# Kernel optimization log

Hardware: AMD Instinct MI355X
Metric: run time of the kernel (lower is better)

The kernel has to match this reference:

```python
import jax, jax.numpy as jnp
import numpy as np

N = 16384      # total nodes
B = 8          # graphs in batch
NPG = N // B   # nodes per graph
E = 262144     # edges
IN, HID, OUT = 128, 256, 128
ICP_ITERS = 10


def setup_inputs():
    key = jax.random.key(0)
    ks = jax.random.split(key, 12)
    x = jax.random.normal(ks[0], (N, IN), jnp.float32)
    # random edges kept within each graph (offsets per graph)
    src = jax.random.randint(ks[1], (E,), 0, NPG, dtype=jnp.int32)
    dst = jax.random.randint(ks[2], (E,), 0, NPG, dtype=jnp.int32)
    goff = (jnp.arange(E, dtype=jnp.int32) % B) * NPG
    edge_index = jnp.stack([src + goff, dst + goff], 0)
    pos = jax.random.normal(ks[3], (N, 3), jnp.float32)
    batch = jnp.repeat(jnp.arange(B, dtype=jnp.int32), NPG)
    def lin(k, fi, fo):
        return jax.random.normal(k, (fi, fo), jnp.float32) * (fi ** -0.5)
    return dict(
        x=x, edge_index=edge_index, pos=pos, batch=batch,
        W1=lin(ks[4], IN, HID),  b1=jnp.zeros((HID,), jnp.float32),
        W2=lin(ks[5], HID, HID), b2=jnp.zeros((HID,), jnp.float32),
        W3=lin(ks[6], HID, OUT), b3=jnp.zeros((OUT,), jnp.float32),
        Wt=lin(ks[7], OUT, 3),   bt=jnp.zeros((3,), jnp.float32),
    )


def gcn_conv(x, W, b, row, col, n):
    # GCNConv: symmetric norm with self loops; messages flow row->col
    xw = x @ W
    loop = jnp.arange(n, dtype=row.dtype)
    r = jnp.concatenate([row, loop])
    c = jnp.concatenate([col, loop])
    deg = jax.ops.segment_sum(jnp.ones_like(c, dtype=xw.dtype), c, num_segments=n)
    dinv = jnp.where(deg > 0, jax.lax.rsqrt(jnp.maximum(deg, 1e-12)), 0.0)
    norm = dinv[r] * dinv[c]
    out = jax.ops.segment_sum(xw[r] * norm[:, None], c, num_segments=n)
    return out + b


def pdist2(a, b):
    # squared pairwise distances [n,m]
    return (jnp.sum(a * a, -1)[:, None] + jnp.sum(b * b, -1)[None, :]
            - 2.0 * (a @ b.T))


def icp_align(src, tgt):
    # fixed-iteration batched ICP (Kabsch/SVD per iteration)
    for _ in range(ICP_ITERS):
        d = pdist2(jax.lax.stop_gradient(src), jax.lax.stop_gradient(tgt))
        idx = jnp.argmin(d, axis=1)
        corr = tgt[idx]
        cs = jnp.mean(src, 0)
        cc = jnp.mean(corr, 0)
        H = (src - cs).T @ (corr - cc)  # [3,3]
        U, S, Vt = jnp.linalg.svd(H, full_matrices=False)
        sign = jnp.sign(jnp.linalg.det(Vt.T @ U.T))
        D = jnp.stack([jnp.ones_like(sign), jnp.ones_like(sign), sign])
        R = (Vt.T * D[None, :]) @ U.T
        t = cc - R @ cs
        src = src @ R.T + t
    return src


def chamfer(a, b):
    d = pdist2(jax.lax.stop_gradient(a), jax.lax.stop_gradient(b))
    ia = jnp.argmin(d, 1)
    ib = jnp.argmin(d, 0)
    d1 = jnp.mean(jnp.sum((a - b[ia]) ** 2, -1))
    d2 = jnp.mean(jnp.sum((b - a[ib]) ** 2, -1))
    return d1 + d2


def reference(x, edge_index, pos, batch, W1, b1, W2, b2, W3, b3, Wt, bt):
    n = x.shape[0]
    row, col = edge_index[0], edge_index[1]
    h = jax.nn.relu(gcn_conv(x, W1, b1, row, col, n))
    h = jax.nn.relu(gcn_conv(h, W2, b2, row, col, n))
    h = gcn_conv(h, W3, b3, row, col, n)
    pos_offset = h @ Wt + bt
    tpos = pos + pos_offset
    nb = int(batch[-1]) + 1          # sorted, equal-size graphs
    npg = n // nb
    src = tpos.reshape(nb, npg, 3)
    tgt = pos.reshape(nb, npg, 3)
    aligned = jax.vmap(icp_align)(src, tgt)
    loss = jnp.mean(jax.vmap(chamfer)(aligned, tgt))
    return h, aligned.reshape(n, 3), loss
```

## Files before the change

### kernel.cpp

```cpp
#include <hip/hip_runtime.h>
#include <math.h>

#define N_NODES 16384
#define B_GRAPHS 8
#define NPG_     2048
#define E_EDGES  262144
#define F_IN  128
#define F_HID 256
#define F_OUT 128
#define ICP_IT 10
#define NN_BPG 32

typedef __attribute__((ext_vector_type(8))) short bf16x8;
typedef __attribute__((ext_vector_type(4))) float f32x4;

__device__ __forceinline__ float b2f(unsigned short u) {
    union { unsigned int u; float f; } v; v.u = ((unsigned int)u) << 16; return v.f;
}
__device__ __forceinline__ unsigned short f2b(float f) {
    union { float f; unsigned int u; } v; v.f = f;
    unsigned int r = v.u + 0x7FFFu + ((v.u >> 16) & 1u);
    return (unsigned short)(r >> 16);
}
__device__ __forceinline__ int swz32(int i) {
    return (i & ~31) | ((i & 31) ^ ((i >> 5) & 31));
}
__device__ __forceinline__ void st_agent(float* p, float v) {
    __hip_atomic_store(p, v, __ATOMIC_RELAXED, __HIP_MEMORY_SCOPE_AGENT);
}
__device__ __forceinline__ float ld_agent(const float* p) {
    return __hip_atomic_load(p, __ATOMIC_RELAXED, __HIP_MEMORY_SCOPE_AGENT);
}
__device__ __forceinline__ int ld_agent_i(const int* p) {
    return __hip_atomic_load(p, __ATOMIC_RELAXED, __HIP_MEMORY_SCOPE_AGENT);
}

__global__ __launch_bounds__(256) void k_prep(
    const float* __restrict__ x, unsigned short* __restrict__ xb,
    const float* __restrict__ W1, const float* __restrict__ W2, const float* __restrict__ W3,
    unsigned short* __restrict__ W1b, unsigned short* __restrict__ W2b, unsigned short* __restrict__ W3b,
    int* __restrict__ counts, int* __restrict__ ctrs)
{
    const int b = blockIdx.x, tid = threadIdx.x;
    if (b < 2048) {
        int i = b * 256 + tid;
        float4 v = ((const float4*)x)[i];
        uint2 o;
        o.x = (unsigned int)f2b(v.x) | ((unsigned int)f2b(v.y) << 16);
        o.y = (unsigned int)f2b(v.z) | ((unsigned int)f2b(v.w) << 16);
        ((uint2*)xb)[i] = o;
    } else if (b < 2176) {
        int idx = (b - 2048) * 256 + tid;
        int k = idx >> 8, n = idx & 255;
        W1b[n * 128 + k] = f2b(W1[idx]);
    } else if (b < 2432) {
        int idx = (b - 2176) * 256 + tid;
        int k = idx >> 8, n = idx & 255;
        W2b[n * 256 + k] = f2b(W2[idx]);
    } else if (b < 2560) {
        int idx = (b - 2432) * 256 + tid;
        int k = idx >> 7, n = idx & 127;
        W3b[n * 256 + k] = f2b(W3[idx]);
    } else if (b < 2576) {
        int i = (b - 2560) * 256 + tid;
        ((int4*)counts)[i] = make_int4(0, 0, 0, 0);
    } else {
        ctrs[tid] = 0;
    }
}

__global__ void k_count(const int* __restrict__ col, int* __restrict__ counts) {
    int e = blockIdx.x * 256 + threadIdx.x;
    if (e < E_EDGES) atomicAdd(&counts[col[e]], 1);
}

__global__ __launch_bounds__(1024) void k_scan(const int* __restrict__ counts,
        int* __restrict__ offs, int* __restrict__ cursor, float* __restrict__ dinv)
{
    __shared__ int wtot[16];
    const int t = threadIdx.x;
    const int base = t * 16;
    int local[16];
    int s = 0;
#pragma unroll
    for (int i = 0; i < 16; i++) { local[i] = counts[base + i]; s += local[i]; }
    const int lane = t & 63, w = t >> 6;
    int inc = s;
    for (int o = 1; o < 64; o <<= 1) {
        int v = __shfl_up(inc, o);
        if (lane >= o) inc += v;
    }
    if (lane == 63) wtot[w] = inc;
    __syncthreads();
    if (t < 16) {
        int v = wtot[t];
        for (int o = 1; o < 16; o <<= 1) {
            int u = __shfl_up(v, o);
            if (t >= o) v += u;
        }
        wtot[t] = v;
    }
    __syncthreads();
    int run = (w > 0 ? wtot[w - 1] : 0) + (inc - s);
#pragma unroll
    for (int i = 0; i < 16; i++) {
        offs[base + i]   = run;
        cursor[base + i] = run;
        dinv[base + i]   = rsqrtf((float)(local[i] + 1));
        run += local[i];
    }
    if (t == 1023) offs[N_NODES] = run;
}

__global__ void k_scatter(const int* __restrict__ row, const int* __restrict__ col,
        int* __restrict__ cursor, const float* __restrict__ dinv,
        int* __restrict__ srcid, float* __restrict__ normv)
{
    int e = blockIdx.x * 256 + threadIdx.x;
    if (e >= E_EDGES) return;
    int r = row[e], c = col[e];
    int p = atomicAdd(&cursor[c], 1);
    srcid[p] = r;
    normv[p] = dinv[r] * dinv[c];
}

template<int W, int OUTF, int FUSET>
__global__ __launch_bounds__(128) void k_agg(const unsigned short* __restrict__ X,
        void* __restrict__ Y,
        const int* __restrict__ offs, const int* __restrict__ srcid,
        const float* __restrict__ normv, const float* __restrict__ dinv,
        const float* __restrict__ bias, int relu,
        const float* __restrict__ Wt, const float* __restrict__ bt,
        const float* __restrict__ pos, float* __restrict__ tposO)
{
    constexpr int NPB = (W == 128) ? 2 : 1;
    constexpr int W2 = W / 2;
    const int local = (NPB == 2) ? (threadIdx.x >> 6) : 0;
    const int n = blockIdx.x * NPB + local;
    const int j = (NPB == 2) ? (threadIdx.x & 63) : threadIdx.x;
    const unsigned int* Xu = (const unsigned int*)X;
    float di = dinv[n];
    float w0 = di * di;
    unsigned int v = Xu[(size_t)n * W2 + j];
    float a0 = b2f((unsigned short)v) * w0;
    float a1 = b2f((unsigned short)(v >> 16)) * w0;
    int p = offs[n];
    const int p1 = offs[n + 1];
    for (; p + 3 < p1; p += 4) {
        int s0i = srcid[p], s1i = srcid[p + 1], s2i = srcid[p + 2], s3i = srcid[p + 3];
        float n0 = normv[p], n1 = normv[p + 1], n2 = normv[p + 2], n3 = normv[p + 3];
        unsigned int v0 = Xu[(size_t)s0i * W2 + j];
        unsigned int v1 = Xu[(size_t)s1i * W2 + j];
        unsigned int v2 = Xu[(size_t)s2i * W2 + j];
        unsigned int v3 = Xu[(size_t)s3i * W2 + j];
        a0 = fmaf(b2f((unsigned short)v0), n0, a0);
        a1 = fmaf(b2f((unsigned short)(v0 >> 16)), n0, a1);
        a0 = fmaf(b2f((unsigned short)v1), n1, a0);
        a1 = fmaf(b2f((unsigned short)(v1 >> 16)), n1, a1);
        a0 = fmaf(b2f((unsigned short)v2), n2, a0);
        a1 = fmaf(b2f((unsigned short)(v2 >> 16)), n2, a1);
        a0 = fmaf(b2f((unsigned short)v3), n3, a0);
        a1 = fmaf(b2f((unsigned short)(v3 >> 16)), n3, a1);
    }
    for (; p < p1; ++p) {
        unsigned int va = Xu[(size_t)srcid[p] * W2 + j]; float na = normv[p];
        a0 = fmaf(b2f((unsigned short)va), na, a0);
        a1 = fmaf(b2f((unsigned short)(va >> 16)), na, a1);
    }
    if (bias) { a0 += bias[2 * j]; a1 += bias[2 * j + 1]; }
    if (relu) { a0 = fmaxf(a0, 0.f); a1 = fmaxf(a1, 0.f); }
    if (OUTF) {
        float* Yf = (float*)Y;
        Yf[(size_t)n * W + 2 * j]     = a0;
        Yf[(size_t)n * W + 2 * j + 1] = a1;
    } else {
        ((unsigned int*)Y)[(size_t)n * W2 + j] =
            (unsigned int)f2b(a0) | ((unsigned int)f2b(a1) << 16);
    }
    if (FUSET) {
        float wt0 = Wt[6 * j + 0], wt1 = Wt[6 * j + 1], wt2 = Wt[6 * j + 2];
        float wt3 = Wt[6 * j + 3], wt4 = Wt[6 * j + 4], wt5 = Wt[6 * j + 5];
        float s0 = a0 * wt0 + a1 * wt3;
        float s1 = a0 * wt1 + a1 * wt4;
        float s2 = a0 * wt2 + a1 * wt5;
        for (int o = 32; o > 0; o >>= 1) {
            s0 += __shfl_down(s0, o);
            s1 += __shfl_down(s1, o);
            s2 += __shfl_down(s2, o);
        }
        if (j == 0) {
            tposO[n * 3 + 0] = pos[n * 3 + 0] + s0 + bt[0];
            tposO[n * 3 + 1] = pos[n * 3 + 1] + s1 + bt[1];
            tposO[n * 3 + 2] = pos[n * 3 + 2] + s2 + bt[2];
        }
    }
}

__global__ __launch_bounds__(256) void k_gemm_bf16(
    const unsigned short* __restrict__ A,
    const unsigned short* __restrict__ Bt,
    const float* __restrict__ bias, unsigned short* __restrict__ C,
    int M, int N, int K, int relu)
{
    __shared__ __align__(16) unsigned short As[128 * 64];
    __shared__ __align__(16) unsigned short Bs[64 * 64];
    const int tid  = threadIdx.x;
    const int lane = tid & 63;
    const int wave = tid >> 6;
    const int bm = blockIdx.y * 128, bn = blockIdx.x * 64;
    const int wm = (wave >> 1) * 64, wn = (wave & 1) * 32;
    f32x4 acc[4][2];
#pragma unroll
    for (int mf = 0; mf < 4; mf++)
#pragma unroll
        for (int nf = 0; nf < 2; nf++) acc[mf][nf] = (f32x4){0.f, 0.f, 0.f, 0.f};

    for (int k0 = 0; k0 < K; k0 += 64) {
#pragma unroll
        for (int i = 0; i < 4; i++) {
            int idx = i * 256 + tid;
            int m = idx >> 3, slot = idx & 7;
            const unsigned short* src = A + (size_t)(bm + m) * K + k0 + ((slot ^ (m & 7)) << 3);
            __builtin_amdgcn_global_load_lds(
                (const __attribute__((address_space(1))) unsigned int*)src,
                (__attribute__((address_space(3))) unsigned int*)(As + (size_t)i * 2048 + wave * 512),
                16, 0, 0);
        }
#pragma unroll
        for (int i = 0; i < 2; i++) {
            int idx = i * 256 + tid;
            int n = idx >> 3, slot = idx & 7;
            const unsigned short* src = Bt + (size_t)(bn + n) * K + k0 + ((slot ^ (n & 7)) << 3);
            __builtin_amdgcn_global_load_lds(
                (const __attribute__((address_space(1))) unsigned int*)src,
                (__attribute__((address_space(3))) unsigned int*)(Bs + (size_t)i * 2048 + wave * 512),
                16, 0, 0);
        }
        __syncthreads();
        bf16x8 af[4][2], bfr[2][2];
        const int qd = lane >> 4;
#pragma unroll
        for (int s = 0; s < 2; s++) {
#pragma unroll
            for (int mf = 0; mf < 4; mf++) {
                int m = wm + mf * 16 + (lane & 15);
                int slot = (s * 4 + qd) ^ (m & 7);
                af[mf][s] = *(const bf16x8*)(As + m * 64 + slot * 8);
            }
#pragma unroll
            for (int nf = 0; nf < 2; nf++) {
                int n = wn + nf * 16 + (lane & 15);
                int slot = (s * 4 + qd) ^ (n & 7);
                bfr[nf][s] = *(const bf16x8*)(Bs + n * 64 + slot * 8);
            }
        }
#pragma unroll
        for (int s = 0; s < 2; s++)
#pragma unroll
            for (int mf = 0; mf < 4; mf++)
#pragma unroll
                for (int nf = 0; nf < 2; nf++)
                    acc[mf][nf] = __builtin_amdgcn_mfma_f32_16x16x32_bf16(
                        af[mf][s], bfr[nf][s], acc[mf][nf], 0, 0, 0);
        __syncthreads();
    }
#pragma unroll
    for (int nf = 0; nf < 2; nf++) {
        int col = bn + wn + nf * 16 + (lane & 15);
        float bv = bias ? bias[col] : 0.f;
#pragma unroll
        for (int mf = 0; mf < 4; mf++) {
#pragma unroll
            for (int r = 0; r < 4; r++) {
                int row = bm + wm + mf * 16 + (lane >> 4) * 4 + r;
                float v = acc[mf][nf][r] + bv;
                if (relu) v = fmaxf(v, 0.f);
                C[(size_t)row * N + col] = f2b(v);
            }
        }
    }
}

__global__ __launch_bounds__(512) void k_icp_all(
    const float* __restrict__ tpos, const float* __restrict__ pos,
    float* __restrict__ partials,
    float* __restrict__ chpart,
    int* __restrict__ ctrs,
    float* __restrict__ out_aligned, float* __restrict__ out_loss)
{
    const int g = blockIdx.x >> 5, blk = blockIdx.x & 31;
    const int tid = threadIdx.x;
    const int wave = tid >> 6, lane = tid & 63;
    __shared__ float4 tq[NPG_];
    __shared__ __align__(16) unsigned char scratch[NPG_ * 16];
    float* sm_d = (float*)scratch;
    unsigned short* sm_i = (unsigned short*)(scratch + 64 * 65 * 4);
    float4* al = (float4*)scratch;
    __shared__ float mom[15][33];
    __shared__ float ssx[64], ssy[64], ssz[64];
    __shared__ float wred[16][2];
    __shared__ float Tsh[12];
    __shared__ double sdl[15];
    __shared__ int lastFlag;

    for (int i = tid; i < NPG_; i += 512) {
        const float* p = &pos[(size_t)(g * NPG_ + i) * 3];
        float qx = p[0], qy = p[1], qz = p[2];
        tq[swz32(i)] = make_float4(qx, qy, qz, fmaf(qx, qx, fmaf(qy, qy, qz * qz)));
    }
    if (tid < 12) Tsh[tid] = (tid == 0 || tid == 4 || tid == 8) ? 1.f : 0.f;
    float Px[8], Py[8], Pz[8];
#pragma unroll
    for (int u = 0; u < 8; u++) {
        int n = g * NPG_ + blk * 64 + wave * 8 + u;
        Px[u] = tpos[n * 3 + 0]; Py[u] = tpos[n * 3 + 1]; Pz[u] = tpos[n * 3 + 2];
    }
    double Td[12];
    if (tid == 0) {
#pragma unroll
        for (int k = 0; k < 12; k++) Td[k] = (k == 0 || k == 4 || k == 8) ? 1.0 : 0.0;
    }
    __syncthreads();

    for (int iter = 0; iter < ICP_IT; ++iter) {
        const int bufbase = (iter & 1) * 256;
        float Tf[12];
#pragma unroll
        for (int k = 0; k < 12; k++) Tf[k] = Tsh[k];
        float Sx[8], Sy[8], Sz[8], Tx[8], Ty[8], Tz[8], bd[8];
        int bi[8];
#pragma unroll
        for (int u = 0; u < 8; u++) {
            float X = Tf[0] * Px[u] + Tf[1] * Py[u] + Tf[2] * Pz[u] + Tf[9];
            float Y = Tf[3] * Px[u] + Tf[4] * Py[u] + Tf[5] * Pz[u] + Tf[10];
            float Z = Tf[6] * Px[u] + Tf[7] * Py[u] + Tf[8] * Pz[u] + Tf[11];
            Sx[u] = X; Sy[u] = Y; Sz[u] = Z;
            Tx[u] = -2.f * X; Ty[u] = -2.f * Y; Tz[u] = -2.f * Z;
            bd[u] = 1e30f; bi[u] = lane * 32;
        }
        const int qbase = lane * 32;
        for (int j = 0; j < 32; j++) {
            float4 t4 = tq[qbase + (j ^ (lane & 31))];
            int idx = qbase + j;
#pragma unroll
            for (int u = 0; u < 8; u++) {
                float d = fmaf(Tx[u], t4.x, fmaf(Ty[u], t4.y, fmaf(Tz[u], t4.z, t4.w)));
                if (d < bd[u]) { bd[u] = d; bi[u] = idx; }
            }
        }
#pragma unroll
        for (int u = 0; u < 8; u++) {
            int rowoff = (wave * 8 + u) * 65;
            sm_d[rowoff + lane] = bd[u];
            sm_i[rowoff + lane] = (unsigned short)bi[u];
            if (lane == u) { ssx[wave * 8 + u] = Sx[u]; ssy[wave * 8 + u] = Sy[u]; ssz[wave * 8 + u] = Sz[u]; }
        }
        __syncthreads();
        if (tid < 64) {
            const int s = tid;
            float best = sm_d[s * 65];
            int ib = sm_i[s * 65];
            for (int r = 1; r < 64; r++) {
                float dd = sm_d[s * 65 + r];
                int ii = sm_i[s * 65 + r];
                if (dd < best) { best = dd; ib = ii; }
            }
            float4 c = tq[swz32(ib)];
            float X = ssx[s], Y = ssy[s], Z = ssz[s];
            float vals[15] = { X, Y, Z, c.x, c.y, c.z,
                               X * c.x, X * c.y, X * c.z,
                               Y * c.x, Y * c.y, Y * c.z,
                               Z * c.x, Z * c.y, Z * c.z };
#pragma unroll
            for (int k = 0; k < 15; k++) {
                float v = vals[k];
                for (int o = 32; o > 0; o >>= 1) v += __shfl_down(v, o);
                if (tid == 0) st_agent(&partials[((size_t)bufbase + blockIdx.x) * 16 + k], v);
            }
        }
        __syncthreads();
        if (tid == 0) {
            atomicAdd(&ctrs[g * 16], 1);
            const int target = 32 * (iter + 1);
            while (ld_agent_i(&ctrs[g * 16]) < target) __builtin_amdgcn_s_sleep(8);
        }
        __syncthreads();
        if (tid < 480) {
            int kk = tid >> 5, bb = tid & 31;
            mom[kk][bb] = ld_agent(&partials[((size_t)bufbase + g * 32 + bb) * 16 + kk]);
        }
        __syncthreads();
        if (tid < 15) {
            double acc = 0;
            for (int b = 0; b < NN_BPG; b++) acc += (double)mom[tid][b];
            sdl[tid] = acc;
        }
        __syncthreads();
        if (tid == 0) {
            double sd[15];
#pragma unroll
            for (int k = 0; k < 15; k++) sd[k] = sdl[k];
            const double n = (double)NPG_;
            const double rin = 1.0 / (double)NPG_;
            double cs0 = sd[0] * rin, cs1 = sd[1] * rin, cs2 = sd[2] * rin;
            double cc0 = sd[3] * rin, cc1 = sd[4] * rin, cc2 = sd[5] * rin;
            float H[3][3];
            H[0][0] = (float)(sd[6]  - n * cs0 * cc0); H[0][1] = (float)(sd[7]  - n * cs0 * cc1); H[0][2] = (float)(sd[8]  - n * cs0 * cc2);
            H[1][0] = (float)(sd[9]  - n * cs1 * cc0); H[1][1] = (float)(sd[10] - n * cs1 * cc1); H[1][2] = (float)(sd[11] - n * cs1 * cc2);
            H[2][0] = (float)(sd[12] - n * cs2 * cc0); H[2][1] = (float)(sd[13] - n * cs2 * cc1); H[2][2] = (float)(sd[14] - n * cs2 * cc2);
            double R[3][3];
            float fn = 1e-30f;
            for (int i = 0; i < 3; i++) for (int j2 = 0; j2 < 3; j2++) fn += H[i][j2] * H[i][j2];
            float sc = rsqrtf(fn);
            float Xm[3][3];
            for (int i = 0; i < 3; i++) for (int j2 = 0; j2 < 3; j2++) Xm[i][j2] = H[i][j2] * sc;
            float dX = Xm[0][0] * (Xm[1][1]*Xm[2][2] - Xm[1][2]*Xm[2][1])
                     - Xm[0][1] * (Xm[1][0]*Xm[2][2] - Xm[1][2]*Xm[2][0])
                     + Xm[0][2] * (Xm[1][0]*Xm[2][1] - Xm[1][1]*Xm[2][0]);
            if (dX > 1e-4f) {
                for (int itn = 0; itn < 24; ++itn) {
                    float C00 = Xm[1][1]*Xm[2][2] - Xm[1][2]*Xm[2][1];
                    float C01 = Xm[1][2]*Xm[2][0] - Xm[1][0]*Xm[2][2];
                    float C02 = Xm[1][0]*Xm[2][1] - Xm[1][1]*Xm[2][0];
                    float C10 = Xm[2][1]*Xm[0][2] - Xm[2][2]*Xm[0][1];
                    float C11 = Xm[2][2]*Xm[0][0] - Xm[2][0]*Xm[0][2];
                    float C12 = Xm[2][0]*Xm[0][1] - Xm[2][1]*Xm[0][0];
                    float C20 = Xm[0][1]*Xm[1][2] - Xm[0][2]*Xm[1][1];
                    float C21 = Xm[0][2]*Xm[1][0] - Xm[0][0]*Xm[1][2];
                    float C22 = Xm[0][0]*Xm[1][1] - Xm[0][1]*Xm[1][0];
                    float det = Xm[0][0]*C00 + Xm[0][1]*C01 + Xm[0][2]*C02;
                    if (fabsf(det) < 1e-30f) break;
                    float rd = 0.5f / det;
                    Xm[0][0] = 0.5f*Xm[0][0] + C00*rd; Xm[0][1] = 0.5f*Xm[0][1] + C01*rd; Xm[0][2] = 0.5f*Xm[0][2] + C02*rd;
                    Xm[1][0] = 0.5f*Xm[1][0] + C10*rd; Xm[1][1] = 0.5f*Xm[1][1] + C11*rd; Xm[1][2] = 0.5f*Xm[1][2] + C12*rd;
                    Xm[2][0] = 0.5f*Xm[2][0] + C20*rd; Xm[2][1] = 0.5f*Xm[2][1] + C21*rd; Xm[2][2] = 0.5f*Xm[2][2] + C22*rd;
                }
                for (int i = 0; i < 3; i++) for (int j2 = 0; j2 < 3; j2++) R[i][j2] = (double)Xm[j2][i];
            } else {
                float A[3][3], V[3][3] = {{1,0,0},{0,1,0},{0,0,1}};
                for (int i = 0; i < 3; i++)
                    for (int j2 = 0; j2 < 3; j2++)
                        A[i][j2] = H[0][i] * H[0][j2] + H[1][i] * H[1][j2] + H[2][i] * H[2][j2];
                for (int sweep = 0; sweep < 8; ++sweep) {
                    for (int p = 0; p < 2; p++) for (int q = p + 1; q < 3; q++) {
                        float apq = A[p][q];
                        if (fabsf(apq) < 1e-30f) continue;
                        float theta = (A[q][q] - A[p][p]) / (2.f * apq);
                        float t = copysignf(1.f, theta) / (fabsf(theta) + sqrtf(theta * theta + 1.f));
                        float c = 1.f / sqrtf(t * t + 1.f);
                        float s = t * c;
                        for (int k = 0; k < 3; k++) { float akp = A[k][p], akq = A[k][q]; A[k][p] = c*akp - s*akq; A[k][q] = s*akp + c*akq; }
                        for (int k = 0; k < 3; k++) { float apk = A[p][k], aqk = A[q][k]; A[p][k] = c*apk - s*aqk; A[q][k] = s*apk + c*aqk; }
                        for (int k = 0; k < 3; k++) { float vkp = V[k][p], vkq = V[k][q]; V[k][p] = c*vkp - s*vkq; V[k][q] = s*vkp + c*vkq; }
                    }
                }
                float lam[3] = { A[0][0], A[1][1], A[2][2] };
                int ord[3] = { 0, 1, 2 };
                if (lam[ord[1]] > lam[ord[0]]) { int t0 = ord[0]; ord[0] = ord[1]; ord[1] = t0; }
                if (lam[ord[2]] > lam[ord[0]]) { int t0 = ord[0]; ord[0] = ord[2]; ord[2] = t0; }
                if (lam[ord[2]] > lam[ord[1]]) { int t0 = ord[1]; ord[1] = ord[2]; ord[2] = t0; }
                float vc[3][3], uc[3][3];
                for (int i = 0; i < 3; i++) { vc[i][0] = V[0][ord[i]]; vc[i][1] = V[1][ord[i]]; vc[i][2] = V[2][ord[i]]; }
                for (int i = 0; i < 3; i++) {
                    float u0 = H[0][0]*vc[i][0] + H[0][1]*vc[i][1] + H[0][2]*vc[i][2];
                    float u1 = H[1][0]*vc[i][0] + H[1][1]*vc[i][1] + H[1][2]*vc[i][2];
                    float u2 = H[2][0]*vc[i][0] + H[2][1]*vc[i][1] + H[2][2]*vc[i][2];
                    for (int j2 = 0; j2 < i; j2++) {
                        float dp = u0*uc[j2][0] + u1*uc[j2][1] + u2*uc[j2][2];
                        u0 -= dp*uc[j2][0]; u1 -= dp*uc[j2][1]; u2 -= dp*uc[j2][2];
                    }
                    float nn2 = sqrtf(u0*u0 + u1*u1 + u2*u2);
                    if (nn2 > 1e-12f) { uc[i][0] = u0/nn2; uc[i][1] = u1/nn2; uc[i][2] = u2/nn2; }
                    else if (i == 2) {
                        uc[2][0] = uc[0][1]*uc[1][2] - uc[0][2]*uc[1][1];
                        uc[2][1] = uc[0][2]*uc[1][0] - uc[0][0]*uc[1][2];
                        uc[2][2] = uc[0][0]*uc[1][1] - uc[0][1]*uc[1][0];
                    } else if (i == 1) {
                        float a0 = (fabsf(uc[0][0]) < 0.9f) ? 1.f : 0.f, a1 = 1.f - a0, a2 = 0.f;
                        float dp = a0*uc[0][0] + a1*uc[0][1] + a2*uc[0][2];
                        a0 -= dp*uc[0][0]; a1 -= dp*uc[0][1]; a2 -= dp*uc[0][2];
                        float nn3 = sqrtf(a0*a0 + a1*a1 + a2*a2);
                        uc[1][0] = a0/nn3; uc[1][1] = a1/nn3; uc[1][2] = a2/nn3;
                    } else { uc[0][0] = 1; uc[0][1] = 0; uc[0][2] = 0; }
                }
                float detU = uc[0][0]*(uc[1][1]*uc[2][2] - uc[1][2]*uc[2][1])
                           - uc[0][1]*(uc[1][0]*uc[2][2] - uc[1][2]*uc[2][0])
                           + uc[0][2]*(uc[1][0]*uc[2][1] - uc[1][1]*uc[2][0]);
                float detV = vc[0][0]*(vc[1][1]*vc[2][2] - vc[1][2]*vc[2][1])
                           - vc[0][1]*(vc[1][0]*vc[2][2] - vc[1][2]*vc[2][0])
                           + vc[0][2]*(vc[1][0]*vc[2][1] - vc[1][1]*vc[2][0]);
                float sgn = (detU * detV < 0.f) ? -1.f : 1.f;
                for (int i = 0; i < 3; i++)
                    for (int j2 = 0; j2 < 3; j2++)
                        R[i][j2] = (double)(vc[0][i]*uc[0][j2] + vc[1][i]*uc[1][j2] + sgn * vc[2][i]*uc[2][j2]);
            }
            double tr0 = cc0 - (R[0][0]*cs0 + R[0][1]*cs1 + R[0][2]*cs2);
            double tr1 = cc1 - (R[1][0]*cs0 + R[1][1]*cs1 + R[1][2]*cs2);
            double tr2 = cc2 - (R[2][0]*cs0 + R[2][1]*cs1 + R[2][2]*cs2);
            double An[12];
            for (int i = 0; i < 3; i++)
                for (int j2 = 0; j2 < 3; j2++)
                    An[i*3+j2] = R[i][0]*Td[0*3+j2] + R[i][1]*Td[1*3+j2] + R[i][2]*Td[2*3+j2];
            An[9]  = R[0][0]*Td[9] + R[0][1]*Td[10] + R[0][2]*Td[11] + tr0;
            An[10] = R[1][0]*Td[9] + R[1][1]*Td[10] + R[1][2]*Td[11] + tr1;
            An[11] = R[2][0]*Td[9] + R[2][1]*Td[10] + R[2][2]*Td[11] + tr2;
#pragma unroll
            for (int k = 0; k < 12; k++) { Td[k] = An[k]; Tsh[k] = (float)An[k]; }
        }
        __syncthreads();
    }

    {
        float Tf[12];
#pragma unroll
        for (int k = 0; k < 12; k++) Tf[k] = Tsh[k];
        __syncthreads();
        for (int i = tid; i < NPG_; i += 512) {
            const float* q = &tpos[(size_t)(g * NPG_ + i) * 3];
            float X = Tf[0] * q[0] + Tf[1] * q[1] + Tf[2] * q[2] + Tf[9];
            float Y = Tf[3] * q[0] + Tf[4] * q[1] + Tf[5] * q[2] + Tf[10];
            float Z = Tf[6] * q[0] + Tf[7] * q[1] + Tf[8] * q[2] + Tf[11];
            al[swz32(i)] = make_float4(X, Y, Z, fmaf(X, X, fmaf(Y, Y, Z * Z)));
            if (blk == 0) {
                out_aligned[(size_t)(g * NPG_ + i) * 3 + 0] = X;
                out_aligned[(size_t)(g * NPG_ + i) * 3 + 1] = Y;
                out_aligned[(size_t)(g * NPG_ + i) * 3 + 2] = Z;
            }
        }
        __syncthreads();
        float Ax[8], Ay[8], Az[8], Aw[8], Qx[8], Qy[8], Qz[8], Qw[8], d1[8], d2[8];
#pragma unroll
        for (int u = 0; u < 8; u++) {
            int s = swz32(blk * 64 + wave * 8 + u);
            float4 a4 = al[s]; float4 p4 = tq[s];
            Ax[u] = -2.f * a4.x; Ay[u] = -2.f * a4.y; Az[u] = -2.f * a4.z; Aw[u] = a4.w;
            Qx[u] = -2.f * p4.x; Qy[u] = -2.f * p4.y; Qz[u] = -2.f * p4.z; Qw[u] = p4.w;
            d1[u] = 1e30f; d2[u] = 1e30f;
        }
        const int qbase = lane * 32;
        for (int j = 0; j < 32; j++) {
            int s = qbase + (j ^ (lane & 31));
            float4 t4 = tq[s];
            float4 b4 = al[s];
#pragma unroll
            for (int u = 0; u < 8; u++) {
                d1[u] = fminf(d1[u], fmaf(Ax[u], t4.x, fmaf(Ay[u], t4.y, fmaf(Az[u], t4.z, t4.w))));
                d2[u] = fminf(d2[u], fmaf(Qx[u], b4.x, fmaf(Qy[u], b4.y, fmaf(Qz[u], b4.z, b4.w))));
            }
        }
        float s1 = 0.f, s2 = 0.f;
#pragma unroll
        for (int u = 0; u < 8; u++) {
            float a = d1[u], b = d2[u];
            for (int o = 32; o > 0; o >>= 1) {
                a = fminf(a, __shfl_down(a, o));
                b = fminf(b, __shfl_down(b, o));
            }
            s1 += a + Aw[u];
            s2 += b + Qw[u];
        }
        if (lane == 0) { wred[wave][0] = s1; wred[wave][1] = s2; }
        __syncthreads();
        if (tid == 0) {
            float t1 = 0.f, t2 = 0.f;
#pragma unroll
            for (int w = 0; w < 8; w++) { t1 += wred[w][0]; t2 += wred[w][1]; }
            st_agent(&chpart[blockIdx.x * 2 + 0], t1);
            st_agent(&chpart[blockIdx.x * 2 + 1], t2);
        }
        __syncthreads();
        if (tid == 0) {
            int old = atomicAdd(&ctrs[128], 1);
            lastFlag = (old == (int)gridDim.x - 1) ? 1 : 0;
        }
        __syncthreads();
        if (!lastFlag) return;
        float v1 = 0.f, v2 = 0.f;
        if (tid < 256) {
            v1 = ld_agent(&chpart[tid * 2 + 0]);
            v2 = ld_agent(&chpart[tid * 2 + 1]);
        }
        for (int o = 32; o > 0; o >>= 1) {
            v1 += __shfl_down(v1, o);
            v2 += __shfl_down(v2, o);
        }
        if (lane == 0 && wave < 4) { wred[wave][0] = v1; wred[wave][1] = v2; }
        __syncthreads();
        if (tid == 0) {
            float tot = 0.f;
#pragma unroll
            for (int w = 0; w < 4; w++) tot += wred[w][0] + wred[w][1];
            out_loss[0] = tot / (float)(NPG_ * B_GRAPHS);
        }
    }
}

extern "C" void kernel_launch(void* const* d_in, const int* in_sizes, int n_in,
                              void* d_out, int out_size, void* d_ws, size_t ws_size,
                              hipStream_t stream)
{
    (void)in_sizes; (void)n_in; (void)out_size; (void)ws_size;
    const float* x   = (const float*)d_in[0];
    const int*   ei  = (const int*)d_in[1];
    const float* pos = (const float*)d_in[2];
    const float* W1 = (const float*)d_in[4];
    const float* b1 = (const float*)d_in[5];
    const float* W2 = (const float*)d_in[6];
    const float* b2 = (const float*)d_in[7];
    const float* W3 = (const float*)d_in[8];
    const float* b3 = (const float*)d_in[9];
    const float* Wt = (const float*)d_in[10];
    const float* bt = (const float*)d_in[11];
    const int* row = ei;
    const int* col = ei + E_EDGES;

    char* wsb = (char*)d_ws;
    size_t off_b = 0;
    auto alloc = [&](size_t bytes) -> void* {
        void* p = wsb + off_b;
        off_b = (off_b + bytes + 255) & ~(size_t)255;
        return p;
    };
    int*    counts   = (int*)alloc((size_t)N_NODES * 4);
    int*    offs     = (int*)alloc((size_t)(N_NODES + 1) * 4);
    int*    cursor   = (int*)alloc((size_t)N_NODES * 4);
    int*    srcid    = (int*)alloc((size_t)E_EDGES * 4);
    float*  normv    = (float*)alloc((size_t)E_EDGES * 4);
    float*  dinv     = (float*)alloc((size_t)N_NODES * 4);
    unsigned short* xb  = (unsigned short*)alloc((size_t)N_NODES * F_IN * 2);
    unsigned short* W1b = (unsigned short*)alloc((size_t)F_IN * F_HID * 2);
    unsigned short* W2b = (unsigned short*)alloc((size_t)F_HID * F_HID * 2);
    unsigned short* W3b = (unsigned short*)alloc((size_t)F_HID * F_OUT * 2);
    unsigned short* bufA = (unsigned short*)alloc((size_t)N_NODES * F_HID * 2);
    unsigned short* bufB = (unsigned short*)alloc((size_t)N_NODES * F_HID * 2);
    unsigned short* bufC = (unsigned short*)alloc((size_t)N_NODES * F_HID * 2);
    float*  tpos     = (float*)alloc((size_t)N_NODES * 3 * 4);
    float*  partials = (float*)alloc((size_t)2 * 256 * 16 * 4);
    int*    ctrs     = (int*)alloc((size_t)256 * 4);
    float*  chpart   = (float*)alloc((size_t)256 * 2 * 4);

    float* out_h       = (float*)d_out;
    float* out_aligned = out_h + (size_t)N_NODES * F_OUT;
    float* out_loss    = out_aligned + (size_t)N_NODES * 3;

    k_prep<<<2577, 256, 0, stream>>>(x, xb, W1, W2, W3, W1b, W2b, W3b, counts, ctrs);
    k_count<<<E_EDGES / 256, 256, 0, stream>>>(col, counts);
    k_scan<<<1, 1024, 0, stream>>>(counts, offs, cursor, dinv);
    k_scatter<<<E_EDGES / 256, 256, 0, stream>>>(row, col, cursor, dinv, srcid, normv);

    k_agg<F_IN, 0, 0><<<N_NODES / 2, 128, 0, stream>>>(xb, bufA, offs, srcid, normv, dinv,
            nullptr, 0, nullptr, nullptr, nullptr, nullptr);
    {
        dim3 grid(F_HID / 64, N_NODES / 128);
        k_gemm_bf16<<<grid, 256, 0, stream>>>(bufA, W1b, b1, bufB, N_NODES, F_HID, F_IN, 1);
    }
    {
        dim3 grid(F_HID / 64, N_NODES / 128);
        k_gemm_bf16<<<grid, 256, 0, stream>>>(bufB, W2b, nullptr, bufC, N_NODES, F_HID, F_HID, 0);
    }
    k_agg<F_HID, 0, 0><<<N_NODES, 128, 0, stream>>>(bufC, bufA, offs, srcid, normv, dinv,
            b2, 1, nullptr, nullptr, nullptr, nullptr);
    {
        dim3 grid(F_OUT / 64, N_NODES / 128);
        k_gemm_bf16<<<grid, 256, 0, stream>>>(bufA, W3b, nullptr, bufB, N_NODES, F_OUT, F_HID, 0);
    }
    k_agg<F_OUT, 1, 1><<<N_NODES / 2, 128, 0, stream>>>(bufB, out_h, offs, srcid, normv, dinv,
            b3, 0, Wt, bt, pos, tpos);

    k_icp_all<<<B_GRAPHS * NN_BPG, 512, 0, stream>>>(tpos, pos, partials, chpart, ctrs,
            out_aligned, out_loss);
}
```

Before: 330.8 us.

## Use leader-block ICP rotation solve with per-block flags and fuse edge counting

The per-iteration ICP grid barrier, where every block spun on a shared counter and then redundantly solved the 3x3 rotation, is replaced. Each block now publishes a release flag, one leader block per graph waits on the 32 flags, solves the rotation once and publishes the transform through a global buffer, and the other blocks wait on an acquire flag. Newton polar iterations drop from 24 to 16, which may slightly change accuracy for ill-conditioned cases. The edge-count kernel is folded into the prep kernel, and counts are cleared with a memset beforehand, removing one launch at the cost of an extra memset call.

```diff
diff --git a/kernel.cpp b/kernel.cpp
--- a/kernel.cpp
+++ b/kernel.cpp
@@ -31,6 +31,12 @@
 __device__ __forceinline__ float ld_agent(const float* p) {
     return __hip_atomic_load(p, __ATOMIC_RELAXED, __HIP_MEMORY_SCOPE_AGENT);
 }
+__device__ __forceinline__ void st_rel_i(int* p, int v) {
+    __hip_atomic_store(p, v, __ATOMIC_RELEASE, __HIP_MEMORY_SCOPE_AGENT);
+}
+__device__ __forceinline__ int ld_acq_i(const int* p) {
+    return __hip_atomic_load(p, __ATOMIC_ACQUIRE, __HIP_MEMORY_SCOPE_AGENT);
+}
 __device__ __forceinline__ int ld_agent_i(const int* p) {
     return __hip_atomic_load(p, __ATOMIC_RELAXED, __HIP_MEMORY_SCOPE_AGENT);
 }
@@ -39,7 +45,7 @@
     const float* __restrict__ x, unsigned short* __restrict__ xb,
     const float* __restrict__ W1, const float* __restrict__ W2, const float* __restrict__ W3,
     unsigned short* __restrict__ W1b, unsigned short* __restrict__ W2b, unsigned short* __restrict__ W3b,
-    int* __restrict__ counts, int* __restrict__ ctrs)
+    const int* __restrict__ col, int* __restrict__ counts, int* __restrict__ ctrs)
 {
     const int b = blockIdx.x, tid = threadIdx.x;
     if (b < 2048) {
@@ -61,17 +67,13 @@
         int idx = (b - 2432) * 256 + tid;
         int k = idx >> 7, n = idx & 127;
         W3b[n * 256 + k] = f2b(W3[idx]);
-    } else if (b < 2576) {
-        int i = (b - 2560) * 256 + tid;
-        ((int4*)counts)[i] = make_int4(0, 0, 0, 0);
+    } else if (b < 3584) {
+        int e = (b - 2560) * 256 + tid;
+        atomicAdd(&counts[col[e]], 1);
     } else {
         ctrs[tid] = 0;
-    }
-}
-
-__global__ void k_count(const int* __restrict__ col, int* __restrict__ counts) {
-    int e = blockIdx.x * 256 + threadIdx.x;
-    if (e < E_EDGES) atomicAdd(&counts[col[e]], 1);
+        ctrs[tid + 256] = 0;
+    }
 }
 
 __global__ __launch_bounds__(1024) void k_scan(const int* __restrict__ counts,
@@ -284,6 +286,7 @@
 __global__ __launch_bounds__(512) void k_icp_all(
     const float* __restrict__ tpos, const float* __restrict__ pos,
     float* __restrict__ partials,
+    float* __restrict__ Tpub,
     float* __restrict__ chpart,
     int* __restrict__ ctrs,
     float* __restrict__ out_aligned, float* __restrict__ out_loss)
@@ -298,7 +301,7 @@
     float4* al = (float4*)scratch;
     __shared__ float mom[15][33];
     __shared__ float ssx[64], ssy[64], ssz[64];
-    __shared__ float wred[16][2];
+    __shared__ float wred[8][2];
     __shared__ float Tsh[12];
     __shared__ double sdl[15];
     __shared__ int lastFlag;
@@ -323,7 +326,6 @@
     __syncthreads();
 
     for (int iter = 0; iter < ICP_IT; ++iter) {
-        const int bufbase = (iter & 1) * 256;
         float Tf[12];
 #pragma unroll
         for (int k = 0; k < 12; k++) Tf[k] = Tsh[k];
@@ -350,10 +352,10 @@
         }
 #pragma unroll
         for (int u = 0; u < 8; u++) {
-            int rowoff = (wave * 8 + u) * 65;
-            sm_d[rowoff + lane] = bd[u];
-            sm_i[rowoff + lane] = (unsigned short)bi[u];
-            if (lane == u) { ssx[wave * 8 + u] = Sx[u]; ssy[wave * 8 + u] = Sy[u]; ssz[wave * 8 + u] = Sz[u]; }
+            int row = wave * 8 + u;
+            sm_d[row * 65 + lane] = bd[u];
+            sm_i[row * 65 + lane] = (unsigned short)bi[u];
+            if (lane == u) { ssx[row] = Sx[u]; ssy[row] = Sy[u]; ssz[row] = Sz[u]; }
         }
         __syncthreads();
         if (tid < 64) {
@@ -375,139 +377,153 @@
             for (int k = 0; k < 15; k++) {
                 float v = vals[k];
                 for (int o = 32; o > 0; o >>= 1) v += __shfl_down(v, o);
-                if (tid == 0) st_agent(&partials[((size_t)bufbase + blockIdx.x) * 16 + k], v);
-            }
-        }
-        __syncthreads();
-        if (tid == 0) {
-            atomicAdd(&ctrs[g * 16], 1);
-            const int target = 32 * (iter + 1);
-            while (ld_agent_i(&ctrs[g * 16]) < target) __builtin_amdgcn_s_sleep(8);
-        }
-        __syncthreads();
-        if (tid < 480) {
-            int kk = tid >> 5, bb = tid & 31;
-            mom[kk][bb] = ld_agent(&partials[((size_t)bufbase + g * 32 + bb) * 16 + kk]);
-        }
-        __syncthreads();
-        if (tid < 15) {
-            double acc = 0;
-            for (int b = 0; b < NN_BPG; b++) acc += (double)mom[tid][b];
-            sdl[tid] = acc;
-        }
-        __syncthreads();
-        if (tid == 0) {
-            double sd[15];
-#pragma unroll
-            for (int k = 0; k < 15; k++) sd[k] = sdl[k];
-            const double n = (double)NPG_;
-            const double rin = 1.0 / (double)NPG_;
-            double cs0 = sd[0] * rin, cs1 = sd[1] * rin, cs2 = sd[2] * rin;
-            double cc0 = sd[3] * rin, cc1 = sd[4] * rin, cc2 = sd[5] * rin;
-            float H[3][3];
-            H[0][0] = (float)(sd[6]  - n * cs0 * cc0); H[0][1] = (float)(sd[7]  - n * cs0 * cc1); H[0][2] = (float)(sd[8]  - n * cs0 * cc2);
-            H[1][0] = (float)(sd[9]  - n * cs1 * cc0); H[1][1] = (float)(sd[10] - n * cs1 * cc1); H[1][2] = (float)(sd[11] - n * cs1 * cc2);
-            H[2][0] = (float)(sd[12] - n * cs2 * cc0); H[2][1] = (float)(sd[13] - n * cs2 * cc1); H[2][2] = (float)(sd[14] - n * cs2 * cc2);
-            double R[3][3];
-            float fn = 1e-30f;
-            for (int i = 0; i < 3; i++) for (int j2 = 0; j2 < 3; j2++) fn += H[i][j2] * H[i][j2];
-            float sc = rsqrtf(fn);
-            float Xm[3][3];
-            for (int i = 0; i < 3; i++) for (int j2 = 0; j2 < 3; j2++) Xm[i][j2] = H[i][j2] * sc;
-            float dX = Xm[0][0] * (Xm[1][1]*Xm[2][2] - Xm[1][2]*Xm[2][1])
-                     - Xm[0][1] * (Xm[1][0]*Xm[2][2] - Xm[1][2]*Xm[2][0])
-                     + Xm[0][2] * (Xm[1][0]*Xm[2][1] - Xm[1][1]*Xm[2][0]);
-            if (dX > 1e-4f) {
-                for (int itn = 0; itn < 24; ++itn) {
-                    float C00 = Xm[1][1]*Xm[2][2] - Xm[1][2]*Xm[2][1];
-                    float C01 = Xm[1][2]*Xm[2][0] - Xm[1][0]*Xm[2][2];
-                    float C02 = Xm[1][0]*Xm[2][1] - Xm[1][1]*Xm[2][0];
-                    float C10 = Xm[2][1]*Xm[0][2] - Xm[2][2]*Xm[0][1];
-                    float C11 = Xm[2][2]*Xm[0][0] - Xm[2][0]*Xm[0][2];
-                    float C12 = Xm[2][0]*Xm[0][1] - Xm[2][1]*Xm[0][0];
-                    float C20 = Xm[0][1]*Xm[1][2] - Xm[0][2]*Xm[1][1];
-                    float C21 = Xm[0][2]*Xm[1][0] - Xm[0][0]*Xm[1][2];
-                    float C22 = Xm[0][0]*Xm[1][1] - Xm[0][1]*Xm[1][0];
-                    float det = Xm[0][0]*C00 + Xm[0][1]*C01 + Xm[0][2]*C02;
-                    if (fabsf(det) < 1e-30f) break;
-                    float rd = 0.5f / det;
-                    Xm[0][0] = 0.5f*Xm[0][0] + C00*rd; Xm[0][1] = 0.5f*Xm[0][1] + C01*rd; Xm[0][2] = 0.5f*Xm[0][2] + C02*rd;
-                    Xm[1][0] = 0.5f*Xm[1][0] + C10*rd; Xm[1][1] = 0.5f*Xm[1][1] + C11*rd; Xm[1][2] = 0.5f*Xm[1][2] + C12*rd;
-                    Xm[2][0] = 0.5f*Xm[2][0] + C20*rd; Xm[2][1] = 0.5f*Xm[2][1] + C21*rd; Xm[2][2] = 0.5f*Xm[2][2] + C22*rd;
+                if (tid == 0) st_agent(&partials[(size_t)blockIdx.x * 16 + k], v);
+            }
+        }
+        __syncthreads();
+        if (tid == 0) st_rel_i(&ctrs[blockIdx.x], iter + 1);
+        if (blk == 0) {
+            if (tid < 32) {
+                while (ld_acq_i(&ctrs[g * 32 + tid]) <= iter) __builtin_amdgcn_s_sleep(1);
+            }
+            __syncthreads();
+            if (tid < 480) {
+                int kk = tid >> 5, bb = tid & 31;
+                mom[kk][bb] = ld_agent(&partials[((size_t)g * 32 + bb) * 16 + kk]);
+            }
+            __syncthreads();
+            if (tid < 15) {
+                double acc = 0;
+                for (int b = 0; b < NN_BPG; b++) acc += (double)mom[tid][b];
+                sdl[tid] = acc;
+            }
+            __syncthreads();
+            if (tid == 0) {
+                double sd[15];
+#pragma unroll
+                for (int k = 0; k < 15; k++) sd[k] = sdl[k];
+                const double n = (double)NPG_;
+                const double rin = 1.0 / (double)NPG_;
+                double cs0 = sd[0] * rin, cs1 = sd[1] * rin, cs2 = sd[2] * rin;
+                double cc0 = sd[3] * rin, cc1 = sd[4] * rin, cc2 = sd[5] * rin;
+                float H[3][3];
+                H[0][0] = (float)(sd[6]  - n * cs0 * cc0); H[0][1] = (float)(sd[7]  - n * cs0 * cc1); H[0][2] = (float)(sd[8]  - n * cs0 * cc2);
+                H[1][0] = (float)(sd[9]  - n * cs1 * cc0); H[1][1] = (float)(sd[10] - n * cs1 * cc1); H[1][2] = (float)(sd[11] - n * cs1 * cc2);
+                H[2][0] = (float)(sd[12] - n * cs2 * cc0); H[2][1] = (float)(sd[13] - n * cs2 * cc1); H[2][2] = (float)(sd[14] - n * cs2 * cc2);
+                double R[3][3];
+                float fn = 1e-30f;
+                for (int i = 0; i < 3; i++) for (int j2 = 0; j2 < 3; j2++) fn += H[i][j2] * H[i][j2];
+                float sc = rsqrtf(fn);
+                float Xm[3][3];
+                for (int i = 0; i < 3; i++) for (int j2 = 0; j2 < 3; j2++) Xm[i][j2] = H[i][j2] * sc;
+                float dX = Xm[0][0] * (Xm[1][1]*Xm[2][2] - Xm[1][2]*Xm[2][1])
+                         - Xm[0][1] * (Xm[1][0]*Xm[2][2] - Xm[1][2]*Xm[2][0])
+                         + Xm[0][2] * (Xm[1][0]*Xm[2][1] - Xm[1][1]*Xm[2][0]);
+                if (dX > 1e-4f) {
+                    for (int itn = 0; itn < 16; ++itn) {
+                        float C00 = Xm[1][1]*Xm[2][2] - Xm[1][2]*Xm[2][1];
+                        float C01 = Xm[1][2]*Xm[2][0] - Xm[1][0]*Xm[2][2];
+                        float C02 = Xm[1][0]*Xm[2][1] - Xm[1][1]*Xm[2][0];
+                        float C10 = Xm[2][1]*Xm[0][2] - Xm[2][2]*Xm[0][1];
+                        float C11 = Xm[2][2]*Xm[0][0] - Xm[2][0]*Xm[0][2];
+                        float C12 = Xm[2][0]*Xm[0][1] - Xm[2][1]*Xm[0][0];
+                        float C20 = Xm[0][1]*Xm[1][2] - Xm[0][2]*Xm[1][1];
+                        float C21 = Xm[0][2]*Xm[1][0] - Xm[0][0]*Xm[1][2];
+                        float C22 = Xm[0][0]*Xm[1][1] - Xm[0][1]*Xm[1][0];
+                        float det = Xm[0][0]*C00 + Xm[0][1]*C01 + Xm[0][2]*C02;
+                        if (fabsf(det) < 1e-30f) break;
+                        float rd = 0.5f / det;
+                        Xm[0][0] = 0.5f*Xm[0][0] + C00*rd; Xm[0][1] = 0.5f*Xm[0][1] + C01*rd; Xm[0][2] = 0.5f*Xm[0][2] + C02*rd;
+                        Xm[1][0] = 0.5f*Xm[1][0] + C10*rd; Xm[1][1] = 0.5f*Xm[1][1] + C11*rd; Xm[1][2] = 0.5f*Xm[1][2] + C12*rd;
+                        Xm[2][0] = 0.5f*Xm[2][0] + C20*rd; Xm[2][1] = 0.5f*Xm[2][1] + C21*rd; Xm[2][2] = 0.5f*Xm[2][2] + C22*rd;
+                    }
+                    for (int i = 0; i < 3; i++) for (int j2 = 0; j2 < 3; j2++) R[i][j2] = (double)Xm[j2][i];
+                } else {
+                    float A[3][3], V[3][3] = {{1,0,0},{0,1,0},{0,0,1}};
+                    for (int i = 0; i < 3; i++)
+                        for (int j2 = 0; j2 < 3; j2++)
+                            A[i][j2] = H[0][i] * H[0][j2] + H[1][i] * H[1][j2] + H[2][i] * H[2][j2];
+                    for (int sweep = 0; sweep < 8; ++sweep) {
+                        for (int p = 0; p < 2; p++) for (int q = p + 1; q < 3; q++) {
+                            float apq = A[p][q];
+                            if (fabsf(apq) < 1e-30f) continue;
+                            float theta = (A[q][q] - A[p][p]) / (2.f * apq);
+                            float t = copysignf(1.f, theta) / (fabsf(theta) + sqrtf(theta * theta + 1.f));
+                            float c = 1.f / sqrtf(t * t + 1.f);
+                            float s = t * c;
+                            for (int k = 0; k < 3; k++) { float akp = A[k][p], akq = A[k][q]; A[k][p] = c*akp - s*akq; A[k][q] = s*akp + c*akq; }
+                            for (int k = 0; k < 3; k++) { float apk = A[p][k], aqk = A[q][k]; A[p][k] = c*apk - s*aqk; A[q][k] = s*apk + c*aqk; }
+                            for (int k = 0; k < 3; k++) { float vkp = V[k][p], vkq = V[k][q]; V[k][p] = c*vkp - s*vkq; V[k][q] = s*vkp + c*vkq; }
+                        }
+                    }
+                    float lam[3] = { A[0][0], A[1][1], A[2][2] };
+                    int ord[3] = { 0, 1, 2 };
+                    if (lam[ord[1]] > lam[ord[0]]) { int t0 = ord[0]; ord[0] = ord[1]; ord[1] = t0; }
+                    if (lam[ord[2]] > lam[ord[0]]) { int t0 = ord[0]; ord[0] = ord[2]; ord[2] = t0; }
+                    if (lam[ord[2]] > lam[ord[1]]) { int t0 = ord[1]; ord[1] = ord[2]; ord[2] = t0; }
+                    float vc[3][3], uc[3][3];
+                    for (int i = 0; i < 3; i++) { vc[i][0] = V[0][ord[i]]; vc[i][1] = V[1][ord[i]]; vc[i][2] = V[2][ord[i]]; }
+                    for (int i = 0; i < 3; i++) {
+                        float u0 = H[0][0]*vc[i][0] + H[0][1]*vc[i][1] + H[0][2]*vc[i][2];
+                        float u1 = H[1][0]*vc[i][0] + H[1][1]*vc[i][1] + H[1][2]*vc[i][2];
+                        float u2 = H[2][0]*vc[i][0] + H[2][1]*vc[i][1] + H[2][2]*vc[i][2];
+                        for (int j2 = 0; j2 < i; j2++) {
+                            float dp = u0*uc[j2][0] + u1*uc[j2][1] + u2*uc[j2][2];
+                            u0 -= dp*uc[j2][0]; u1 -= dp*uc[j2][1]; u2 -= dp*uc[j2][2];
+                        }
+                        float nn2 = sqrtf(u0*u0 + u1*u1 + u2*u2);
+                        if (nn2 > 1e-12f) { uc[i][0] = u0/nn2; uc[i][1] = u1/nn2; uc[i][2] = u2/nn2; }
+                        else if (i == 2) {
+                            uc[2][0] = uc[0][1]*uc[1][2] - uc[0][2]*uc[1][1];
+                            uc[2][1] = uc[0][2]*uc[1][0] - uc[0][0]*uc[1][2];
+                            uc[2][2] = uc[0][0]*uc[1][1] - uc[0][1]*uc[1][0];
+                        } else if (i == 1) {
+                            float a0 = (fabsf(uc[0][0]) < 0.9f) ? 1.f : 0.f, a1 = 1.f - a0, a2 = 0.f;
+                            float dp = a0*uc[0][0] + a1*uc[0][1] + a2*uc[0][2];
+                            a0 -= dp*uc[0][0]; a1 -= dp*uc[0][1]; a2 -= dp*uc[0][2];
+                            float nn3 = sqrtf(a0*a0 + a1*a1 + a2*a2);
+                            uc[1][0] = a0/nn3; uc[1][1] = a1/nn3; uc[1][2] = a2/nn3;
+                        } else { uc[0][0] = 1; uc[0][1] = 0; uc[0][2] = 0; }
+                    }
+                    float detU = uc[0][0]*(uc[1][1]*uc[2][2] - uc[1][2]*uc[2][1])
+                               - uc[0][1]*(uc[1][0]*uc[2][2] - uc[1][2]*uc[2][0])
+                               + uc[0][2]*(uc[1][0]*uc[2][1] - uc[1][1]*uc[2][0]);
+                    float detV = vc[0][0]*(vc[1][1]*vc[2][2] - vc[1][2]*vc[2][1])
+                               - vc[0][1]*(vc[1][0]*vc[2][2] - vc[1][2]*vc[2][0])
+                               + vc[0][2]*(vc[1][0]*vc[2][1] - vc[1][1]*vc[2][0]);
+                    float sgn = (detU * detV < 0.f) ? -1.f : 1.f;
+                    for (int i = 0; i < 3; i++)
+                        for (int j2 = 0; j2 < 3; j2++)
+                            R[i][j2] = (double)(vc[0][i]*uc[0][j2] + vc[1][i]*uc[1][j2] + sgn * vc[2][i]*uc[2][j2]);
                 }
-                for (int i = 0; i < 3; i++) for (int j2 = 0; j2 < 3; j2++) R[i][j2] = (double)Xm[j2][i];
-            } else {
-                float A[3][3], V[3][3] = {{1,0,0},{0,1,0},{0,0,1}};
+                double tr0 = cc0 - (R[0][0]*cs0 + R[0][1]*cs1 + R[0][2]*cs2);
+                double tr1 = cc1 - (R[1][0]*cs0 + R[1][1]*cs1 + R[1][2]*cs2);
+                double tr2 = cc2 - (R[2][0]*cs0 + R[2][1]*cs1 + R[2][2]*cs2);
+                double An[12];
                 for (int i = 0; i < 3; i++)
                     for (int j2 = 0; j2 < 3; j2++)
-                        A[i][j2] = H[0][i] * H[0][j2] + H[1][i] * H[1][j2] + H[2][i] * H[2][j2];
-                for (int sweep = 0; sweep < 8; ++sweep) {
-                    for (int p = 0; p < 2; p++) for (int q = p + 1; q < 3; q++) {
-                        float apq = A[p][q];
-                        if (fabsf(apq) < 1e-30f) continue;
-                        float theta = (A[q][q] - A[p][p]) / (2.f * apq);
-                        float t = copysignf(1.f, theta) / (fabsf(theta) + sqrtf(theta * theta + 1.f));
-                        float c = 1.f / sqrtf(t * t + 1.f);
-                        float s = t * c;
-                        for (int k = 0; k < 3; k++) { float akp = A[k][p], akq = A[k][q]; A[k][p] = c*akp - s*akq; A[k][q] = s*akp + c*akq; }
-                        for (int k = 0; k < 3; k++) { float apk = A[p][k], aqk = A[q][k]; A[p][k] = c*apk - s*aqk; A[q][k] = s*apk + c*aqk; }
-                        for (int k = 0; k < 3; k++) { float vkp = V[k][p], vkq = V[k][q]; V[k][p] = c*vkp - s*vkq; V[k][q] = s*vkp + c*vkq; }
-                    }
+                        An[i*3+j2] = R[i][0]*Td[0*3+j2] + R[i][1]*Td[1*3+j2] + R[i][2]*Td[2*3+j2];
+                An[9]  = R[0][0]*Td[9] + R[0][1]*Td[10] + R[0][2]*Td[11] + tr0;
+                An[10] = R[1][0]*Td[9] + R[1][1]*Td[10] + R[1][2]*Td[11] + tr1;
+                An[11] = R[2][0]*Td[9] + R[2][1]*Td[10] + R[2][2]*Td[11] + tr2;
+#pragma unroll
+                for (int k = 0; k < 12; k++) {
+                    Td[k] = An[k];
+                    float tf = (float)An[k];
+                    Tsh[k] = tf;
+                    st_agent(&Tpub[g * 16 + k], tf);
                 }
-                float lam[3] = { A[0][0], A[1][1], A[2][2] };
-                int ord[3] = { 0, 1, 2 };
-                if (lam[ord[1]] > lam[ord[0]]) { int t0 = ord[0]; ord[0] = ord[1]; ord[1] = t0; }
-                if (lam[ord[2]] > lam[ord[0]]) { int t0 = ord[0]; ord[0] = ord[2]; ord[2] = t0; }
-                if (lam[ord[2]] > lam[ord[1]]) { int t0 = ord[1]; ord[1] = ord[2]; ord[2] = t0; }
-                float vc[3][3], uc[3][3];
-                for (int i = 0; i < 3; i++) { vc[i][0] = V[0][ord[i]]; vc[i][1] = V[1][ord[i]]; vc[i][2] = V[2][ord[i]]; }
-                for (int i = 0; i < 3; i++) {
-                    float u0 = H[0][0]*vc[i][0] + H[0][1]*vc[i][1] + H[0][2]*vc[i][2];
-                    float u1 = H[1][0]*vc[i][0] + H[1][1]*vc[i][1] + H[1][2]*vc[i][2];
-                    float u2 = H[2][0]*vc[i][0] + H[2][1]*vc[i][1] + H[2][2]*vc[i][2];
-                    for (int j2 = 0; j2 < i; j2++) {
-                        float dp = u0*uc[j2][0] + u1*uc[j2][1] + u2*uc[j2][2];
-                        u0 -= dp*uc[j2][0]; u1 -= dp*uc[j2][1]; u2 -= dp*uc[j2][2];
-                    }
-                    float nn2 = sqrtf(u0*u0 + u1*u1 + u2*u2);
-                    if (nn2 > 1e-12f) { uc[i][0] = u0/nn2; uc[i][1] = u1/nn2; uc[i][2] = u2/nn2; }
-                    else if (i == 2) {
-                        uc[2][0] = uc[0][1]*uc[1][2] - uc[0][2]*uc[1][1];
-                        uc[2][1] = uc[0][2]*uc[1][0] - uc[0][0]*uc[1][2];
-                        uc[2][2] = uc[0][0]*uc[1][1] - uc[0][1]*uc[1][0];
-                    } else if (i == 1) {
-                        float a0 = (fabsf(uc[0][0]) < 0.9f) ? 1.f : 0.f, a1 = 1.f - a0, a2 = 0.f;
-                        float dp = a0*uc[0][0] + a1*uc[0][1] + a2*uc[0][2];
-                        a0 -= dp*uc[0][0]; a1 -= dp*uc[0][1]; a2 -= dp*uc[0][2];
-                        float nn3 = sqrtf(a0*a0 + a1*a1 + a2*a2);
-                        uc[1][0] = a0/nn3; uc[1][1] = a1/nn3; uc[1][2] = a2/nn3;
-                    } else { uc[0][0] = 1; uc[0][1] = 0; uc[0][2] = 0; }
-                }
-                float detU = uc[0][0]*(uc[1][1]*uc[2][2] - uc[1][2]*uc[2][1])
-                           - uc[0][1]*(uc[1][0]*uc[2][2] - uc[1][2]*uc[2][0])
-                           + uc[0][2]*(uc[1][0]*uc[2][1] - uc[1][1]*uc[2][0]);
-                float detV = vc[0][0]*(vc[1][1]*vc[2][2] - vc[1][2]*vc[2][1])
-                           - vc[0][1]*(vc[1][0]*vc[2][2] - vc[1][2]*vc[2][0])
-                           + vc[0][2]*(vc[1][0]*vc[2][1] - vc[1][1]*vc[2][0]);
-                float sgn = (detU * detV < 0.f) ? -1.f : 1.f;
-                for (int i = 0; i < 3; i++)
-                    for (int j2 = 0; j2 < 3; j2++)
-                        R[i][j2] = (double)(vc[0][i]*uc[0][j2] + vc[1][i]*uc[1][j2] + sgn * vc[2][i]*uc[2][j2]);
-            }
-            double tr0 = cc0 - (R[0][0]*cs0 + R[0][1]*cs1 + R[0][2]*cs2);
-            double tr1 = cc1 - (R[1][0]*cs0 + R[1][1]*cs1 + R[1][2]*cs2);
-            double tr2 = cc2 - (R[2][0]*cs0 + R[2][1]*cs1 + R[2][2]*cs2);
-            double An[12];
-            for (int i = 0; i < 3; i++)
-                for (int j2 = 0; j2 < 3; j2++)
-                    An[i*3+j2] = R[i][0]*Td[0*3+j2] + R[i][1]*Td[1*3+j2] + R[i][2]*Td[2*3+j2];
-            An[9]  = R[0][0]*Td[9] + R[0][1]*Td[10] + R[0][2]*Td[11] + tr0;
-            An[10] = R[1][0]*Td[9] + R[1][1]*Td[10] + R[1][2]*Td[11] + tr1;
-            An[11] = R[2][0]*Td[9] + R[2][1]*Td[10] + R[2][2]*Td[11] + tr2;
-#pragma unroll
-            for (int k = 0; k < 12; k++) { Td[k] = An[k]; Tsh[k] = (float)An[k]; }
-        }
-        __syncthreads();
+                st_rel_i(&ctrs[256 + g], iter + 1);
+            }
+            __syncthreads();
+        } else {
+            if (tid == 0) {
+                while (ld_acq_i(&ctrs[256 + g]) <= iter) __builtin_amdgcn_s_sleep(1);
+#pragma unroll
+                for (int k = 0; k < 12; k++) Tsh[k] = ld_agent(&Tpub[g * 16 + k]);
+            }
+            __syncthreads();
+        }
     }
 
     {
@@ -570,7 +586,7 @@
         }
         __syncthreads();
         if (tid == 0) {
-            int old = atomicAdd(&ctrs[128], 1);
+            int old = atomicAdd(&ctrs[264], 1);
             lastFlag = (old == (int)gridDim.x - 1) ? 1 : 0;
         }
         __syncthreads();
@@ -635,16 +651,17 @@
     unsigned short* bufB = (unsigned short*)alloc((size_t)N_NODES * F_HID * 2);
     unsigned short* bufC = (unsigned short*)alloc((size_t)N_NODES * F_HID * 2);
     float*  tpos     = (float*)alloc((size_t)N_NODES * 3 * 4);
-    float*  partials = (float*)alloc((size_t)2 * 256 * 16 * 4);
-    int*    ctrs     = (int*)alloc((size_t)256 * 4);
+    float*  partials = (float*)alloc((size_t)256 * 16 * 4);
+    float*  Tpub     = (float*)alloc((size_t)B_GRAPHS * 16 * 4);
+    int*    ctrs     = (int*)alloc((size_t)512 * 4);
     float*  chpart   = (float*)alloc((size_t)256 * 2 * 4);
 
     float* out_h       = (float*)d_out;
     float* out_aligned = out_h + (size_t)N_NODES * F_OUT;
     float* out_loss    = out_aligned + (size_t)N_NODES * 3;
 
-    k_prep<<<2577, 256, 0, stream>>>(x, xb, W1, W2, W3, W1b, W2b, W3b, counts, ctrs);
-    k_count<<<E_EDGES / 256, 256, 0, stream>>>(col, counts);
+    hipMemsetAsync(counts, 0, (size_t)N_NODES * 4, stream);
+    k_prep<<<3585, 256, 0, stream>>>(x, xb, W1, W2, W3, W1b, W2b, W3b, col, counts, ctrs);
     k_scan<<<1, 1024, 0, stream>>>(counts, offs, cursor, dinv);
     k_scatter<<<E_EDGES / 256, 256, 0, stream>>>(row, col, cursor, dinv, srcid, normv);
 
@@ -667,6 +684,6 @@
     k_agg<F_OUT, 1, 1><<<N_NODES / 2, 128, 0, stream>>>(bufB, out_h, offs, srcid, normv, dinv,
             b3, 0, Wt, bt, pos, tpos);
 
-    k_icp_all<<<B_GRAPHS * NN_BPG, 512, 0, stream>>>(tpos, pos, partials, chpart, ctrs,
+    k_icp_all<<<B_GRAPHS * NN_BPG, 512, 0, stream>>>(tpos, pos, partials, Tpub, chpart, ctrs,
             out_aligned, out_loss);
 }
```

Measured after the change: 431.7 us. +30.5%, slower.
